# Kernel optimization log

Hardware: AMD Instinct MI355X
Metric: run time of the kernel (lower is better)

The kernel has to match this reference:

```python
import jax, jax.numpy as jnp
import numpy as np

N, C, H, W = 8, 256, 100, 252
TOPK_RATIO = 0.1
CLUSTER_RATIO = 0.125
KNN_K = 10


def setup_inputs() -> dict:
    key = jax.random.key(0)
    ks = jax.random.split(key, 4)
    x = jax.random.normal(ks[0], (N, C, H, W), jnp.float32)
    w1 = jax.random.normal(ks[1], (C, C), jnp.float32) * (1.0 / np.sqrt(C))
    b1 = jnp.zeros((C,), jnp.float32)
    w2 = jax.random.normal(ks[2], (C,), jnp.float32) * (1.0 / np.sqrt(C))
    b2 = jnp.zeros((1,), jnp.float32)
    dis_priority = jnp.ones((N, H, W), jnp.float32)
    record_len = jnp.array([4, 4], dtype=jnp.int32)
    return {"x": x, "w1": w1, "b1": b1, "w2": w2, "b2": b2,
            "dis_priority": dis_priority, "record_len": record_len}


def _layernorm(t, eps=1e-5):
    mu = jnp.mean(t, -1, keepdims=True)
    var = jnp.var(t, -1, keepdims=True)
    return (t - mu) / jnp.sqrt(var + eps)


def reference(x, w1, b1, w2, b2, dis_priority, record_len):
    HW = H * W
    S = int(HW * TOPK_RATIO)                       # sampled tokens per CAV
    K = max(int(np.ceil(S * CLUSTER_RATIO)), 1)    # DPC-KNN cluster count

    xf = x.reshape(N, C, HW)
    # SortSampler: 2layer-fc-256 score net (1x1 convs == per-pixel MLP)
    h1 = jax.nn.relu(jnp.einsum('nch,dc->ndh', xf, w1) + b1[None, :, None])
    score = jax.nn.sigmoid(jnp.einsum('nch,c->nh', h1, w2) + b2)   # [N,HW]
    score = score * dis_priority.reshape(N, HW)

    conf_topk, topk_idx = jax.lax.top_k(score, S)  # descending-sort top-k
    tokens = jnp.take_along_axis(xf, topk_idx[:, None, :], axis=2)  # [N,C,S]
    tokens = _layernorm(tokens.transpose(0, 2, 1))                  # [N,S,C]
    tokens = tokens * conf_topk[..., None]

    # --- cluster_dpc_knn (TCFormer-style DPC-KNN) ---
    sq = jnp.sum(tokens * tokens, -1)
    d2 = sq[:, :, None] + sq[:, None, :] - 2.0 * jnp.einsum('bsc,btc->bst', tokens, tokens)
    dist = jnp.sqrt(jnp.maximum(d2, 1e-12)) / np.sqrt(C)            # [N,S,S]
    neg_near, _ = jax.lax.top_k(-dist, KNN_K)                       # k nearest
    density = jnp.exp(-jnp.mean(neg_near * neg_near, -1))
    density = density + jax.random.uniform(jax.random.key(1), density.shape) * 1e-6
    mask = density[:, None, :] > density[:, :, None]
    dist_max = dist.max(axis=(1, 2), keepdims=True)
    parent_dist = jnp.where(mask, dist, dist_max).min(-1)           # [N,S]
    cscore = parent_dist * density
    _, index_down = jax.lax.top_k(cscore, K)                        # [N,K]
    dist_c = jnp.take_along_axis(dist, index_down[:, :, None], axis=1)  # [N,K,S]
    idx_cluster = jnp.argmin(dist_c, axis=1)                        # [N,S]
    bidx = jnp.arange(N)[:, None]
    idx_cluster = idx_cluster.at[bidx, index_down].set(jnp.arange(K)[None, :])

    # --- merge_tokens: confidence-weighted average per cluster ---
    flat_idx = (idx_cluster + jnp.arange(N)[:, None] * K).reshape(-1)
    wgt = conf_topk.reshape(-1)
    all_w = jax.ops.segment_sum(wgt, flat_idx, num_segments=N * K) + 1e-6
    norm_w = (wgt / all_w[flat_idx])[:, None]
    merged = jax.ops.segment_sum(tokens.reshape(-1, C) * norm_w, flat_idx,
                                 num_segments=N * K).reshape(N, K, C)

    # index_points: broadcast cluster token back to its members
    src = jnp.take_along_axis(merged, idx_cluster[..., None], axis=1)  # [N,S,C]

    # scatter sampled tokens into dense spatial grid
    out = jnp.zeros((N, C, HW), x.dtype)
    out = out.at[bidx, :, topk_idx].set(src)       # [N,S] adv idx -> [N,S,C]

    # ego CAV (first in each record group) keeps full-resolution features
    starts = jnp.concatenate([jnp.zeros((1,), jnp.int32),
                              jnp.cumsum(record_len)[:-1].astype(jnp.int32)])
    is_ego = jnp.zeros((N,), bool).at[starts].set(True)
    out = jnp.where(is_ego[:, None, None], xf, out)
    return out.reshape(N, C, H, W)
```

## Files before the change

### kernel.cpp

```cpp
#include <hip/hip_runtime.h>
#include <cstdio>
#include <cstdint>

#define NN  8
#define CCH 256
#define HWP 25200
#define SS  2520
#define KCL 315
#define KNN 10

__device__ __forceinline__ unsigned fmap(float f) {
  unsigned u = __float_as_uint(f);
  return (u & 0x80000000u) ? ~u : (u | 0x80000000u);
}
__device__ __forceinline__ float funmap(unsigned u) {
  unsigned b = (u & 0x80000000u) ? (u & 0x7fffffffu) : ~u;
  return __uint_as_float(b);
}

__global__ __launch_bounds__(256) void k_w1t(const float* __restrict__ w1, float* __restrict__ w1T) {
  __shared__ float tile[32][33];
  const int bx = blockIdx.x * 32, by = blockIdx.y * 32;
  const int tx = threadIdx.x, ty = threadIdx.y;
  for (int r = 0; r < 32; r += 8)
    tile[ty + r][tx] = w1[(by + ty + r) * CCH + bx + tx];
  __syncthreads();
  for (int r = 0; r < 32; r += 8)
    w1T[(bx + ty + r) * CCH + by + tx] = tile[tx][ty + r];
}

__global__ __launch_bounds__(256) void k_score(
    const float* __restrict__ x, const float* __restrict__ w1T,
    const float* __restrict__ b1, const float* __restrict__ w2,
    const float* __restrict__ b2, const float* __restrict__ pri,
    float* __restrict__ scores)
{
  __shared__ float Wl[16 * 256];
  __shared__ float Xl[16 * 64];
  __shared__ float red[64 * 33];
  const int n = blockIdx.y, p0 = blockIdx.x * 64, tid = threadIdx.x;
  const int dt = tid & 31, pt = tid >> 5;
  float acc[8][8];
#pragma unroll
  for (int i = 0; i < 8; ++i)
#pragma unroll
    for (int j = 0; j < 8; ++j) acc[i][j] = 0.f;

  for (int c0 = 0; c0 < CCH; c0 += 16) {
    {
      const float4* src = (const float4*)(w1T + (size_t)c0 * CCH);
      float4* dst = (float4*)Wl;
#pragma unroll
      for (int i = 0; i < 4; ++i) dst[tid + 256 * i] = src[tid + 256 * i];
    }
    {
      int kk = tid >> 4, q = tid & 15;
      int gp = p0 + 4 * q; if (gp > HWP - 4) gp = HWP - 4;
      *(float4*)&Xl[kk * 64 + 4 * q] = *(const float4*)&x[(size_t)(n * CCH + c0 + kk) * HWP + gp];
    }
    __syncthreads();
#pragma unroll
    for (int kk = 0; kk < 16; ++kk) {
      const float4 w0 = *(const float4*)&Wl[kk * 256 + 4 * dt];
      const float4 w1v = *(const float4*)&Wl[kk * 256 + 128 + 4 * dt];
      const float4 x0 = *(const float4*)&Xl[kk * 64 + 4 * pt];
      const float4 x1 = *(const float4*)&Xl[kk * 64 + 32 + 4 * pt];
      const float a[8] = {w0.x, w0.y, w0.z, w0.w, w1v.x, w1v.y, w1v.z, w1v.w};
      const float b[8] = {x0.x, x0.y, x0.z, x0.w, x1.x, x1.y, x1.z, x1.w};
#pragma unroll
      for (int di = 0; di < 8; ++di)
#pragma unroll
        for (int pj = 0; pj < 8; ++pj) acc[di][pj] += a[di] * b[pj];
    }
    __syncthreads();
  }
  float part[8];
#pragma unroll
  for (int pj = 0; pj < 8; ++pj) part[pj] = 0.f;
#pragma unroll
  for (int di = 0; di < 8; ++di) {
    int d = (di < 4) ? (4 * dt + di) : (128 + 4 * dt + di - 4);
    float bb = b1[d], wv = w2[d];
#pragma unroll
    for (int pj = 0; pj < 8; ++pj) {
      float h = acc[di][pj] + bb; h = h > 0.f ? h : 0.f;
      part[pj] += h * wv;
    }
  }
#pragma unroll
  for (int pj = 0; pj < 8; ++pj) {
    int px = (pj < 4) ? (4 * pt + pj) : (32 + 4 * pt + pj - 4);
    red[px * 33 + dt] = part[pj];
  }
  __syncthreads();
  if (tid < 64) {
    float s = b2[0];
#pragma unroll
    for (int g = 0; g < 32; ++g) s += red[tid * 33 + g];
    float sc = 1.f / (1.f + expf(-s));
    int p = p0 + tid;
    if (p < HWP) scores[n * HWP + p] = sc * pri[n * HWP + p];
  }
}

__device__ __forceinline__ void bitonic4096_desc(unsigned long long* keys, int tid) {
  for (int k = 2; k <= 4096; k <<= 1) {
    for (int j = k >> 1; j > 0; j >>= 1) {
      for (int i = tid; i < 4096; i += 1024) {
        int ixj = i ^ j;
        if (ixj > i) {
          unsigned long long a = keys[i], b = keys[ixj];
          bool up = ((i & k) == 0);
          if ((a < b) == up) { keys[i] = b; keys[ixj] = a; }
        }
      }
      __syncthreads();
    }
  }
}

__global__ __launch_bounds__(1024) void k_topk_sample(
    const float* __restrict__ scores, int* __restrict__ topk_idx, float* __restrict__ conf)
{
  __shared__ unsigned hist[256];
  __shared__ unsigned long long keys[4096];
  __shared__ unsigned sh_rank, sh_chosen;
  __shared__ int sh_cnt;
  const int n = blockIdx.x;
  const int tid = threadIdx.x;
  if (tid == 0) sh_rank = SS;
  __syncthreads();
  unsigned prefix = 0, pmask = 0;
  for (int shift = 24; shift >= 0; shift -= 8) {
    for (int b = tid; b < 256; b += 1024) hist[b] = 0;
    __syncthreads();
    for (int e = tid; e < HWP; e += 1024) {
      unsigned u = fmap(scores[n * HWP + e]);
      if ((u & pmask) == prefix) atomicAdd(&hist[(u >> shift) & 255u], 1u);
    }
    __syncthreads();
    if (tid == 0) {
      unsigned r = sh_rank, chosen = 0;
      for (int b = 255; b >= 0; --b) {
        unsigned cb = hist[b];
        if (cb < r) r -= cb; else { chosen = (unsigned)b; break; }
      }
      sh_rank = r; sh_chosen = chosen;
    }
    __syncthreads();
    prefix |= sh_chosen << shift;
    pmask  |= 0xFFu << shift;
    __syncthreads();
  }
  const unsigned uT = prefix;
  if (tid == 0) sh_cnt = 0;
  for (int i = tid; i < 4096; i += 1024) keys[i] = 0ULL;
  __syncthreads();
  for (int e = tid; e < HWP; e += 1024) {
    unsigned u = fmap(scores[n * HWP + e]);
    if (u >= uT) {
      int s = atomicAdd(&sh_cnt, 1);
      if (s < 4096) keys[s] = ((unsigned long long)u << 32) | (unsigned)(~(unsigned)e);
    }
  }
  __syncthreads();
  bitonic4096_desc(keys, tid);
  for (int t = tid; t < SS; t += 1024) {
    unsigned long long kv = keys[t];
    topk_idx[n * SS + t] = (int)(~(unsigned)kv);
    conf[n * SS + t] = funmap((unsigned)(kv >> 32));
  }
}

__device__ __forceinline__ float block_sum256(float v, float* scratch) {
#pragma unroll
  for (int o = 32; o > 0; o >>= 1) v += __shfl_down(v, o);
  int wid = threadIdx.x >> 6, lane = threadIdx.x & 63;
  if (lane == 0) scratch[wid] = v;
  __syncthreads();
  float r = scratch[0] + scratch[1] + scratch[2] + scratch[3];
  __syncthreads();
  return r;
}

__global__ __launch_bounds__(256) void k_gather_ln(
    const float* __restrict__ x, const int* __restrict__ topk_idx,
    const float* __restrict__ conf, float* __restrict__ tokens, float* __restrict__ sq)
{
  __shared__ float scratch[4];
  const int t = blockIdx.x, n = blockIdx.y, c = threadIdx.x;
  const int p = topk_idx[n * SS + t];
  float v = x[(size_t)(n * CCH + c) * HWP + p];
  float mu = block_sum256(v, scratch) * (1.f / CCH);
  float d = v - mu;
  float var = block_sum256(d * d, scratch) * (1.f / CCH);
  float inv = 1.f / sqrtf(var + 1e-5f);
  float tok = d * inv * conf[n * SS + t];
  tokens[(size_t)(n * SS + t) * CCH + c] = tok;
  float s2 = block_sum256(tok * tok, scratch);
  if (c == 0) sq[n * SS + t] = s2;
}

__global__ __launch_bounds__(256) void k_ttrans(
    const float* __restrict__ tokens, float* __restrict__ tokensT)
{
  __shared__ float tile[64][68];
  const int n = blockIdx.z, t0 = blockIdx.x * 64, cc0 = blockIdx.y * 64;
  const int tid = threadIdx.x;
  for (int l = tid; l < 1024; l += 256) {
    int tr = l >> 4, q = l & 15;
    int gt = t0 + tr;
    float4 v = {0.f, 0.f, 0.f, 0.f};
    if (gt < SS) v = *(const float4*)&tokens[(size_t)(n * SS + gt) * CCH + cc0 + 4 * q];
    *(float4*)&tile[tr][4 * q] = v;
  }
  __syncthreads();
  for (int l = tid; l < 1024; l += 256) {
    int cr = l >> 4, q = l & 15;
    int gt = t0 + 4 * q;
    if (gt <= SS - 4) {
      float4 v;
      v.x = tile[4 * q + 0][cr]; v.y = tile[4 * q + 1][cr];
      v.z = tile[4 * q + 2][cr]; v.w = tile[4 * q + 3][cr];
      *(float4*)&tokensT[(size_t)(n * CCH + cc0 + cr) * SS + gt] = v;
    }
  }
}

__global__ __launch_bounds__(256) void k_gram(
    const float* __restrict__ tokensT, const float* __restrict__ sq,
    float* __restrict__ d2, int* __restrict__ d2max)
{
  const int bi = blockIdx.y, bj = blockIdx.x, n = blockIdx.z;
  if (bj < bi) return;
  __shared__ float Al[16 * 128], Bl[16 * 128];
  __shared__ float redm[256];
  const int i0 = bi * 128, j0 = bj * 128, tid = threadIdx.x;
  const int ti = tid & 15, tj = tid >> 4;
  float acc[8][8];
#pragma unroll
  for (int i = 0; i < 8; ++i)
#pragma unroll
    for (int j = 0; j < 8; ++j) acc[i][j] = 0.f;

  for (int c0 = 0; c0 < CCH; c0 += 16) {
#pragma unroll
    for (int l0 = 0; l0 < 2; ++l0) {
      int l = threadIdx.x + 256 * l0;
      int kk = l >> 5, q = l & 31;
      size_t srow = (size_t)(n * CCH + c0 + kk) * SS;
      float4 z = {0.f, 0.f, 0.f, 0.f};
      int gi = i0 + 4 * q;
      *(float4*)&Al[kk * 128 + 4 * q] = (gi <= SS - 4) ? *(const float4*)&tokensT[srow + gi] : z;
      int gj = j0 + 4 * q;
      *(float4*)&Bl[kk * 128 + 4 * q] = (gj <= SS - 4) ? *(const float4*)&tokensT[srow + gj] : z;
    }
    __syncthreads();
#pragma unroll
    for (int kk = 0; kk < 16; ++kk) {
      const float4 a0 = *(const float4*)&Al[kk * 128 + 4 * ti];
      const float4 a1 = *(const float4*)&Al[kk * 128 + 64 + 4 * ti];
      const float4 b0 = *(const float4*)&Bl[kk * 128 + 4 * tj];
      const float4 b1 = *(const float4*)&Bl[kk * 128 + 64 + 4 * tj];
      const float a[8] = {a0.x, a0.y, a0.z, a0.w, a1.x, a1.y, a1.z, a1.w};
      const float b[8] = {b0.x, b0.y, b0.z, b0.w, b1.x, b1.y, b1.z, b1.w};
#pragma unroll
      for (int ii = 0; ii < 8; ++ii)
#pragma unroll
        for (int jj = 0; jj < 8; ++jj) acc[ii][jj] += a[ii] * b[jj];
    }
    __syncthreads();
  }
  int gi[8], gj[8];
  float sqi[8], sqj[8];
#pragma unroll
  for (int ii = 0; ii < 8; ++ii) {
    gi[ii] = i0 + ((ii < 4) ? (4 * ti + ii) : (64 + 4 * ti + ii - 4));
    sqi[ii] = (gi[ii] < SS) ? sq[n * SS + gi[ii]] : 0.f;
    gj[ii] = j0 + ((ii < 4) ? (4 * tj + ii) : (64 + 4 * tj + ii - 4));
    sqj[ii] = (gj[ii] < SS) ? sq[n * SS + gj[ii]] : 0.f;
  }
  float outv[8][8];
  float mx = -3e38f;
#pragma unroll
  for (int ii = 0; ii < 8; ++ii)
#pragma unroll
    for (int jj = 0; jj < 8; ++jj) {
      float o = sqi[ii] + sqj[jj] - 2.f * acc[ii][jj];
      outv[ii][jj] = o;
      if (gi[ii] < SS && gj[jj] < SS) mx = fmaxf(mx, o);
    }
#pragma unroll
  for (int ii = 0; ii < 8; ++ii) {
    if (gi[ii] < SS) {
      size_t row = (size_t)(n * SS + gi[ii]) * SS;
      int jb0 = j0 + 4 * tj;
      float4 o0 = {outv[ii][0], outv[ii][1], outv[ii][2], outv[ii][3]};
      *(float4*)&d2[row + jb0] = o0;
      int jb1 = j0 + 64 + 4 * tj;
      if (jb1 < SS) {
        float4 o1 = {outv[ii][4], outv[ii][5], outv[ii][6], outv[ii][7]};
        *(float4*)&d2[row + jb1] = o1;
      }
    }
  }
  if (bi != bj) {
#pragma unroll
    for (int jj = 0; jj < 8; ++jj) {
      if (gj[jj] < SS) {
        size_t row = (size_t)(n * SS + gj[jj]) * SS;
        int ib0 = i0 + 4 * ti;
        float4 m0 = {outv[0][jj], outv[1][jj], outv[2][jj], outv[3][jj]};
        *(float4*)&d2[row + ib0] = m0;
        int ib1 = i0 + 64 + 4 * ti;
        if (ib1 < SS) {
          float4 m1 = {outv[4][jj], outv[5][jj], outv[6][jj], outv[7][jj]};
          *(float4*)&d2[row + ib1] = m1;
        }
      }
    }
  }
  redm[tid] = mx; __syncthreads();
  for (int s = 128; s > 0; s >>= 1) {
    if (tid < s) redm[tid] = fmaxf(redm[tid], redm[tid + s]);
    __syncthreads();
  }
  if (tid == 0) atomicMax(&d2max[n], __float_as_int(redm[0]));
}

__global__ __launch_bounds__(256) void k_knn(
    const float* __restrict__ d2, float* __restrict__ density)
{
  const int n = blockIdx.y;
  const int w = threadIdx.x >> 6, lane = threadIdx.x & 63;
  const int i = blockIdx.x * 4 + w;
  const float* dr = &d2[(size_t)(n * SS + i) * SS];
  float s[KNN];
#pragma unroll
  for (int k = 0; k < KNN; ++k) s[k] = 3e38f;
  for (int e = lane; e < SS; e += 64) {
    float t = dr[e];
#pragma unroll
    for (int k = 0; k < KNN; ++k) {
      float lo = fminf(s[k], t);
      t = fmaxf(s[k], t);
      s[k] = lo;
    }
  }
  float sum = 0.f;
  for (int r = 0; r < KNN; ++r) {
    float m = s[0];
#pragma unroll
    for (int o = 32; o > 0; o >>= 1) m = fminf(m, __shfl_xor(m, o));
    unsigned long long msk = __ballot(s[0] == m);
    int first = __ffsll(msk) - 1;
    if (lane == first) {
#pragma unroll
      for (int k = 0; k < KNN - 1; ++k) s[k] = s[k + 1];
      s[KNN - 1] = 3e38f;
    }
    sum += fmaxf(m, 1e-12f);
  }
  if (lane == 0) density[n * SS + i] = expf(-sum * (1.f / (KNN * CCH)));
}

__global__ __launch_bounds__(256) void k_parent(
    const float* __restrict__ d2, const float* __restrict__ density,
    const int* __restrict__ d2max, float* __restrict__ cscore)
{
  __shared__ float swv[4];
  const int i = blockIdx.x, n = blockIdx.y, tid = threadIdx.x;
  const float di = density[n * SS + i];
  const float* dr = &d2[(size_t)(n * SS + i) * SS];
  float m = 3e38f;
  for (int e = tid; e < SS; e += 256) {
    float dj = density[n * SS + e];
    float v = dr[e];
    if (dj > di && v < m) m = v;
  }
#pragma unroll
  for (int o = 32; o > 0; o >>= 1) m = fminf(m, __shfl_down(m, o));
  int wid = tid >> 6, lane = tid & 63;
  if (lane == 0) swv[wid] = m;
  __syncthreads();
  if (tid == 0) {
    float mm = fminf(fminf(swv[0], swv[1]), fminf(swv[2], swv[3]));
    mm = fminf(mm, __int_as_float(d2max[n]));
    float pd = sqrtf(fmaxf(mm, 1e-12f)) * 0.0625f;
    cscore[n * SS + i] = pd * di;
  }
}

__global__ __launch_bounds__(1024) void k_topk_centers(
    const float* __restrict__ cscore, int* __restrict__ index_down)
{
  __shared__ unsigned long long keys[4096];
  const int n = blockIdx.x, tid = threadIdx.x;
  for (int i = tid; i < 4096; i += 1024) {
    unsigned long long kv = 0ULL;
    if (i < SS) kv = ((unsigned long long)fmap(cscore[n * SS + i]) << 32) | (unsigned)(~(unsigned)i);
    keys[i] = kv;
  }
  __syncthreads();
  bitonic4096_desc(keys, tid);
  for (int t = tid; t < KCL; t += 1024)
    index_down[n * KCL + t] = (int)(~(unsigned)keys[t]);
}

__global__ __launch_bounds__(256) void k_assign(
    const float* __restrict__ d2, const int* __restrict__ index_down,
    int* __restrict__ idx_cluster)
{
  const int n = blockIdx.y;
  const int i = blockIdx.x * 256 + threadIdx.x;
  if (i >= SS) return;
  float best = 3e38f; int bk = 0;
  for (int k = 0; k < KCL; ++k) {
    int r = index_down[n * KCL + k];
    float v = d2[(size_t)(n * SS + r) * SS + i];
    if (v < best) { best = v; bk = k; }
  }
  idx_cluster[n * SS + i] = bk;
}

__global__ void k_center_overwrite(const int* __restrict__ index_down, int* __restrict__ idx_cluster) {
  const int n = blockIdx.x; const int k = threadIdx.x;
  if (k < KCL) idx_cluster[n * SS + index_down[n * KCL + k]] = k;
}

__global__ __launch_bounds__(256) void k_weights(
    const int* __restrict__ idx_cluster, const float* __restrict__ conf, float* __restrict__ all_w)
{
  const int n = blockIdx.y; const int i = blockIdx.x * 256 + threadIdx.x;
  if (i >= SS) return;
  atomicAdd(&all_w[n * KCL + idx_cluster[n * SS + i]], conf[n * SS + i]);
}

__global__ __launch_bounds__(256) void k_merge(
    const int* __restrict__ idx_cluster, const float* __restrict__ conf,
    const float* __restrict__ all_w, const float* __restrict__ tokens, float* __restrict__ merged)
{
  const int t = blockIdx.x, n = blockIdx.y, c = threadIdx.x;
  const int k = idx_cluster[n * SS + t];
  const float w = conf[n * SS + t] / (all_w[n * KCL + k] + 1e-6f);
  atomicAdd(&merged[(size_t)(n * KCL + k) * CCH + c],
            tokens[(size_t)(n * SS + t) * CCH + c] * w);
}

__global__ __launch_bounds__(256) void k_kmap(
    const int* __restrict__ topk_idx, const int* __restrict__ idx_cluster, int* __restrict__ kmap)
{
  const int n = blockIdx.y; const int i = blockIdx.x * 256 + threadIdx.x;
  if (i >= SS) return;
  kmap[n * HWP + topk_idx[n * SS + i]] = idx_cluster[n * SS + i];
}

__global__ void k_ego(const int* __restrict__ record_len, int R, int* __restrict__ ego) {
  if (threadIdx.x == 0 && blockIdx.x == 0) {
    int acc = 0;
    for (int r = 0; r < R; ++r) {
      if (acc >= 0 && acc < NN) ego[acc] = 1;
      acc += record_len[r];
    }
  }
}

__global__ __launch_bounds__(256) void k_output(
    const float* __restrict__ x, const float* __restrict__ merged,
    const int* __restrict__ kmap, const int* __restrict__ ego, float* __restrict__ out)
{
  const int n = blockIdx.z, c = blockIdx.y;
  const int p4 = blockIdx.x * 256 + threadIdx.x;
  if (p4 >= HWP / 4) return;
  const size_t base = (size_t)(n * CCH + c) * HWP + 4 * p4;
  float4 v;
  if (ego[n]) {
    v = *(const float4*)&x[base];
  } else {
    int4 k4 = *(const int4*)&kmap[n * HWP + 4 * p4];
    const float* mb = &merged[(size_t)n * KCL * CCH + c];
    v.x = (k4.x >= 0) ? mb[(size_t)k4.x * CCH] : 0.f;
    v.y = (k4.y >= 0) ? mb[(size_t)k4.y * CCH] : 0.f;
    v.z = (k4.z >= 0) ? mb[(size_t)k4.z * CCH] : 0.f;
    v.w = (k4.w >= 0) ? mb[(size_t)k4.w * CCH] : 0.f;
  }
  *(float4*)&out[base] = v;
}

extern "C" void kernel_launch(void* const* d_in, const int* in_sizes, int n_in,
                              void* d_out, int out_size, void* d_ws, size_t ws_size,
                              hipStream_t stream)
{
  const float* x   = (const float*)d_in[0];
  const float* w1  = (const float*)d_in[1];
  const float* b1  = (const float*)d_in[2];
  const float* w2  = (const float*)d_in[3];
  const float* b2  = (const float*)d_in[4];
  const float* pri = (const float*)d_in[5];
  const int*   rec = (const int*)d_in[6];
  const int R = in_sizes[6];
  float* out = (float*)d_out;

  char* ws = (char*)d_ws;
  size_t off = 0;
  auto alloc = [&](size_t bytes) -> char* {
    char* p = ws + off;
    off = (off + bytes + 255) & ~(size_t)255;
    return p;
  };
  float* scores      = (float*)alloc(sizeof(float) * NN * HWP);
  int*   topk_idx    = (int*)  alloc(sizeof(int)   * NN * SS);
  float* conf        = (float*)alloc(sizeof(float) * NN * SS);
  float* tokens      = (float*)alloc(sizeof(float) * (size_t)NN * SS * CCH);
  float* tokensT     = (float*)alloc(sizeof(float) * (size_t)NN * CCH * SS);
  float* w1T         = (float*)alloc(sizeof(float) * CCH * CCH);
  float* sq          = (float*)alloc(sizeof(float) * NN * SS);
  float* density     = (float*)alloc(sizeof(float) * NN * SS);
  float* cscore      = (float*)alloc(sizeof(float) * NN * SS);
  int*   d2max       = (int*)  alloc(sizeof(int)   * NN);
  int*   index_down  = (int*)  alloc(sizeof(int)   * NN * KCL);
  int*   idx_cluster = (int*)  alloc(sizeof(int)   * NN * SS);
  float* all_w       = (float*)alloc(sizeof(float) * NN * KCL);
  float* merged      = (float*)alloc(sizeof(float) * (size_t)NN * KCL * CCH);
  int*   kmap        = (int*)  alloc(sizeof(int)   * NN * HWP);
  int*   ego         = (int*)  alloc(sizeof(int)   * NN);
  float* d2          = (float*)alloc(sizeof(float) * (size_t)NN * SS * SS);
  if (off > ws_size)
    fprintf(stderr, "ERMVP kernel: workspace too small: need %zu, have %zu\n", off, ws_size);

  hipMemsetAsync(d2max, 0, sizeof(int) * NN, stream);
  hipMemsetAsync(all_w, 0, sizeof(float) * NN * KCL, stream);
  hipMemsetAsync(merged, 0, sizeof(float) * (size_t)NN * KCL * CCH, stream);
  hipMemsetAsync(kmap, 0xFF, sizeof(int) * NN * HWP, stream);
  hipMemsetAsync(ego, 0, sizeof(int) * NN, stream);

  k_w1t<<<dim3(8, 8), dim3(32, 8), 0, stream>>>(w1, w1T);
  k_score<<<dim3((HWP + 63) / 64, NN), 256, 0, stream>>>(x, w1T, b1, w2, b2, pri, scores);
  k_topk_sample<<<NN, 1024, 0, stream>>>(scores, topk_idx, conf);
  k_gather_ln<<<dim3(SS, NN), 256, 0, stream>>>(x, topk_idx, conf, tokens, sq);
  k_ttrans<<<dim3((SS + 63) / 64, CCH / 64, NN), 256, 0, stream>>>(tokens, tokensT);
  k_gram<<<dim3(20, 20, NN), 256, 0, stream>>>(tokensT, sq, d2, d2max);
  k_knn<<<dim3(SS / 4, NN), 256, 0, stream>>>(d2, density);
  k_parent<<<dim3(SS, NN), 256, 0, stream>>>(d2, density, d2max, cscore);
  k_topk_centers<<<NN, 1024, 0, stream>>>(cscore, index_down);
  k_assign<<<dim3((SS + 255) / 256, NN), 256, 0, stream>>>(d2, index_down, idx_cluster);
  k_center_overwrite<<<NN, 320, 0, stream>>>(index_down, idx_cluster);
  k_weights<<<dim3((SS + 255) / 256, NN), 256, 0, stream>>>(idx_cluster, conf, all_w);
  k_merge<<<dim3(SS, NN), 256, 0, stream>>>(idx_cluster, conf, all_w, tokens, merged);
  k_kmap<<<dim3((SS + 255) / 256, NN), 256, 0, stream>>>(topk_idx, idx_cluster, kmap);
  k_ego<<<1, 64, 0, stream>>>(rec, R, ego);
  k_output<<<dim3((HWP / 4 + 255) / 256, CCH, NN), 256, 0, stream>>>(x, merged, kmap, ego, out);
}
```

Baseline: 1.267 ms.

## Replace bitonic sorts with radix-select compaction and fuse small clustering kernels

Both top-k kernels now skip the full 4096-element bitonic sort. They find the k-th threshold with the existing radix histogram passes, then compact the selected elements in index order using ballot/popcount prefix sums, with tie-breaking handled explicitly. The sampler also stages the score row in dynamic LDS so the histogram passes do not reread global memory. The center overwrite, weight accumulation and kmap scatter are folded into k_assign, and the ego flag is computed inline in k_output, which removes four small launches and a memset. Selected tokens and centers now come out in index order rather than score order; this relies on later stages being invariant to that permutation, apart from possible argmin tie-breaking differences.

```diff
diff --git a/kernel.cpp b/kernel.cpp
--- a/kernel.cpp
+++ b/kernel.cpp
@@ -12,10 +12,6 @@
 __device__ __forceinline__ unsigned fmap(float f) {
   unsigned u = __float_as_uint(f);
   return (u & 0x80000000u) ? ~u : (u | 0x80000000u);
-}
-__device__ __forceinline__ float funmap(unsigned u) {
-  unsigned b = (u & 0x80000000u) ? (u & 0x7fffffffu) : ~u;
-  return __uint_as_float(b);
 }
 
 __global__ __launch_bounds__(256) void k_w1t(const float* __restrict__ w1, float* __restrict__ w1T) {
@@ -103,39 +99,31 @@
   }
 }
 
-__device__ __forceinline__ void bitonic4096_desc(unsigned long long* keys, int tid) {
-  for (int k = 2; k <= 4096; k <<= 1) {
-    for (int j = k >> 1; j > 0; j >>= 1) {
-      for (int i = tid; i < 4096; i += 1024) {
-        int ixj = i ^ j;
-        if (ixj > i) {
-          unsigned long long a = keys[i], b = keys[ixj];
-          bool up = ((i & k) == 0);
-          if ((a < b) == up) { keys[i] = b; keys[ixj] = a; }
-        }
-      }
-      __syncthreads();
-    }
-  }
-}
-
 __global__ __launch_bounds__(1024) void k_topk_sample(
     const float* __restrict__ scores, int* __restrict__ topk_idx, float* __restrict__ conf)
 {
+  extern __shared__ float sc_lds[];
   __shared__ unsigned hist[256];
-  __shared__ unsigned long long keys[4096];
+  __shared__ int wcnt[16], woff[16];
+  __shared__ int sh_base, sh_tbase, sh_ngt;
   __shared__ unsigned sh_rank, sh_chosen;
-  __shared__ int sh_cnt;
-  const int n = blockIdx.x;
-  const int tid = threadIdx.x;
-  if (tid == 0) sh_rank = SS;
-  __syncthreads();
+  const int n = blockIdx.x, tid = threadIdx.x;
+  const int lane = tid & 63, w = tid >> 6;
+
+  {
+    const float4* src = (const float4*)(scores + (size_t)n * HWP);
+    float4* dst = (float4*)sc_lds;
+    for (int i = tid; i < HWP / 4; i += 1024) dst[i] = src[i];
+  }
+  if (tid == 0) { sh_rank = SS; sh_ngt = 0; sh_base = 0; sh_tbase = 0; }
+  __syncthreads();
+
   unsigned prefix = 0, pmask = 0;
   for (int shift = 24; shift >= 0; shift -= 8) {
-    for (int b = tid; b < 256; b += 1024) hist[b] = 0;
+    if (tid < 256) hist[tid] = 0;
     __syncthreads();
     for (int e = tid; e < HWP; e += 1024) {
-      unsigned u = fmap(scores[n * HWP + e]);
+      unsigned u = fmap(sc_lds[e]);
       if ((u & pmask) == prefix) atomicAdd(&hist[(u >> shift) & 255u], 1u);
     }
     __syncthreads();
@@ -153,22 +141,50 @@
     __syncthreads();
   }
   const unsigned uT = prefix;
-  if (tid == 0) sh_cnt = 0;
-  for (int i = tid; i < 4096; i += 1024) keys[i] = 0ULL;
-  __syncthreads();
-  for (int e = tid; e < HWP; e += 1024) {
-    unsigned u = fmap(scores[n * HWP + e]);
-    if (u >= uT) {
-      int s = atomicAdd(&sh_cnt, 1);
-      if (s < 4096) keys[s] = ((unsigned long long)u << 32) | (unsigned)(~(unsigned)e);
-    }
-  }
-  __syncthreads();
-  bitonic4096_desc(keys, tid);
-  for (int t = tid; t < SS; t += 1024) {
-    unsigned long long kv = keys[t];
-    topk_idx[n * SS + t] = (int)(~(unsigned)kv);
-    conf[n * SS + t] = funmap((unsigned)(kv >> 32));
+
+  {
+    int myg = 0;
+    for (int e = tid; e < HWP; e += 1024) myg += (fmap(sc_lds[e]) > uT);
+#pragma unroll
+    for (int o = 32; o > 0; o >>= 1) myg += __shfl_down(myg, o);
+    if (lane == 0) atomicAdd(&sh_ngt, myg);
+  }
+  __syncthreads();
+  const int T = SS - sh_ngt;
+
+  for (int c0 = 0; c0 < HWP; c0 += 1024) {
+    const int e = c0 + tid;
+    const bool valid = e < HWP;
+    const float s = valid ? sc_lds[e] : 0.f;
+    const unsigned u = valid ? fmap(s) : 0u;
+    const bool tie = valid && (u == uT);
+    const bool gt  = valid && (u > uT);
+    unsigned long long mt = __ballot(tie);
+    if (lane == 0) wcnt[w] = __popcll(mt);
+    __syncthreads();
+    if (tid == 0) {
+      int run = sh_tbase;
+      for (int q = 0; q < 16; ++q) { woff[q] = run; run += wcnt[q]; }
+      sh_tbase = run;
+    }
+    __syncthreads();
+    const int trank = woff[w] + __popcll(mt & ((1ULL << lane) - 1ULL));
+    const bool sel = gt || (tie && trank < T);
+    unsigned long long ms = __ballot(sel);
+    if (lane == 0) wcnt[w] = __popcll(ms);
+    __syncthreads();
+    if (tid == 0) {
+      int run = sh_base;
+      for (int q = 0; q < 16; ++q) { woff[q] = run; run += wcnt[q]; }
+      sh_base = run;
+    }
+    __syncthreads();
+    if (sel) {
+      int pos = woff[w] + __popcll(ms & ((1ULL << lane) - 1ULL));
+      topk_idx[n * SS + pos] = e;
+      conf[n * SS + pos] = s;
+    }
+    __syncthreads();
   }
 }
 
@@ -394,46 +410,105 @@
 __global__ __launch_bounds__(1024) void k_topk_centers(
     const float* __restrict__ cscore, int* __restrict__ index_down)
 {
-  __shared__ unsigned long long keys[4096];
+  __shared__ float cs_lds[SS];
+  __shared__ unsigned hist[256];
+  __shared__ int wcnt[16], woff[16];
+  __shared__ int sh_base, sh_tbase, sh_ngt;
+  __shared__ unsigned sh_rank, sh_chosen;
   const int n = blockIdx.x, tid = threadIdx.x;
-  for (int i = tid; i < 4096; i += 1024) {
-    unsigned long long kv = 0ULL;
-    if (i < SS) kv = ((unsigned long long)fmap(cscore[n * SS + i]) << 32) | (unsigned)(~(unsigned)i);
-    keys[i] = kv;
-  }
-  __syncthreads();
-  bitonic4096_desc(keys, tid);
-  for (int t = tid; t < KCL; t += 1024)
-    index_down[n * KCL + t] = (int)(~(unsigned)keys[t]);
+  const int lane = tid & 63, w = tid >> 6;
+
+  for (int e = tid; e < SS; e += 1024) cs_lds[e] = cscore[n * SS + e];
+  if (tid == 0) { sh_rank = KCL; sh_ngt = 0; sh_base = 0; sh_tbase = 0; }
+  __syncthreads();
+
+  unsigned prefix = 0, pmask = 0;
+  for (int shift = 24; shift >= 0; shift -= 8) {
+    if (tid < 256) hist[tid] = 0;
+    __syncthreads();
+    for (int e = tid; e < SS; e += 1024) {
+      unsigned u = fmap(cs_lds[e]);
+      if ((u & pmask) == prefix) atomicAdd(&hist[(u >> shift) & 255u], 1u);
+    }
+    __syncthreads();
+    if (tid == 0) {
+      unsigned r = sh_rank, chosen = 0;
+      for (int b = 255; b >= 0; --b) {
+        unsigned cb = hist[b];
+        if (cb < r) r -= cb; else { chosen = (unsigned)b; break; }
+      }
+      sh_rank = r; sh_chosen = chosen;
+    }
+    __syncthreads();
+    prefix |= sh_chosen << shift;
+    pmask  |= 0xFFu << shift;
+    __syncthreads();
+  }
+  const unsigned uT = prefix;
+
+  {
+    int myg = 0;
+    for (int e = tid; e < SS; e += 1024) myg += (fmap(cs_lds[e]) > uT);
+#pragma unroll
+    for (int o = 32; o > 0; o >>= 1) myg += __shfl_down(myg, o);
+    if (lane == 0) atomicAdd(&sh_ngt, myg);
+  }
+  __syncthreads();
+  const int T = KCL - sh_ngt;
+
+  for (int c0 = 0; c0 < SS; c0 += 1024) {
+    const int e = c0 + tid;
+    const bool valid = e < SS;
+    const unsigned u = valid ? fmap(cs_lds[e]) : 0u;
+    const bool tie = valid && (u == uT);
+    const bool gt  = valid && (u > uT);
+    unsigned long long mt = __ballot(tie);
+    if (lane == 0) wcnt[w] = __popcll(mt);
+    __syncthreads();
+    if (tid == 0) {
+      int run = sh_tbase;
+      for (int q = 0; q < 16; ++q) { woff[q] = run; run += wcnt[q]; }
+      sh_tbase = run;
+    }
+    __syncthreads();
+    const int trank = woff[w] + __popcll(mt & ((1ULL << lane) - 1ULL));
+    const bool sel = gt || (tie && trank < T);
+    unsigned long long ms = __ballot(sel);
+    if (lane == 0) wcnt[w] = __popcll(ms);
+    __syncthreads();
+    if (tid == 0) {
+      int run = sh_base;
+      for (int q = 0; q < 16; ++q) { woff[q] = run; run += wcnt[q]; }
+      sh_base = run;
+    }
+    __syncthreads();
+    if (sel) {
+      int pos = woff[w] + __popcll(ms & ((1ULL << lane) - 1ULL));
+      index_down[n * KCL + pos] = e;
+    }
+    __syncthreads();
+  }
 }
 
 __global__ __launch_bounds__(256) void k_assign(
     const float* __restrict__ d2, const int* __restrict__ index_down,
-    int* __restrict__ idx_cluster)
+    const float* __restrict__ conf, const int* __restrict__ topk_idx,
+    int* __restrict__ idx_cluster, float* __restrict__ all_w, int* __restrict__ kmap)
 {
   const int n = blockIdx.y;
   const int i = blockIdx.x * 256 + threadIdx.x;
   if (i >= SS) return;
-  float best = 3e38f; int bk = 0;
+  float best = 3e38f; int bk = 0, forced = -1;
   for (int k = 0; k < KCL; ++k) {
     int r = index_down[n * KCL + k];
+    if (r == i) forced = k;
     float v = d2[(size_t)(n * SS + r) * SS + i];
     if (v < best) { best = v; bk = k; }
   }
+  if (forced >= 0) bk = forced;
   idx_cluster[n * SS + i] = bk;
-}
-
-__global__ void k_center_overwrite(const int* __restrict__ index_down, int* __restrict__ idx_cluster) {
-  const int n = blockIdx.x; const int k = threadIdx.x;
-  if (k < KCL) idx_cluster[n * SS + index_down[n * KCL + k]] = k;
-}
-
-__global__ __launch_bounds__(256) void k_weights(
-    const int* __restrict__ idx_cluster, const float* __restrict__ conf, float* __restrict__ all_w)
-{
-  const int n = blockIdx.y; const int i = blockIdx.x * 256 + threadIdx.x;
-  if (i >= SS) return;
-  atomicAdd(&all_w[n * KCL + idx_cluster[n * SS + i]], conf[n * SS + i]);
+  atomicAdd(&all_w[n * KCL + bk], conf[n * SS + i]);
+  kmap[n * HWP + topk_idx[n * SS + i]] = bk;
 }
 
 __global__ __launch_bounds__(256) void k_merge(
@@ -447,34 +522,22 @@
             tokens[(size_t)(n * SS + t) * CCH + c] * w);
 }
 
-__global__ __launch_bounds__(256) void k_kmap(
-    const int* __restrict__ topk_idx, const int* __restrict__ idx_cluster, int* __restrict__ kmap)
-{
-  const int n = blockIdx.y; const int i = blockIdx.x * 256 + threadIdx.x;
-  if (i >= SS) return;
-  kmap[n * HWP + topk_idx[n * SS + i]] = idx_cluster[n * SS + i];
-}
-
-__global__ void k_ego(const int* __restrict__ record_len, int R, int* __restrict__ ego) {
-  if (threadIdx.x == 0 && blockIdx.x == 0) {
-    int acc = 0;
-    for (int r = 0; r < R; ++r) {
-      if (acc >= 0 && acc < NN) ego[acc] = 1;
-      acc += record_len[r];
-    }
-  }
-}
-
 __global__ __launch_bounds__(256) void k_output(
     const float* __restrict__ x, const float* __restrict__ merged,
-    const int* __restrict__ kmap, const int* __restrict__ ego, float* __restrict__ out)
+    const int* __restrict__ kmap, const int* __restrict__ rec, int R,
+    float* __restrict__ out)
 {
   const int n = blockIdx.z, c = blockIdx.y;
   const int p4 = blockIdx.x * 256 + threadIdx.x;
   if (p4 >= HWP / 4) return;
+  bool ego = false;
+  {
+    int acc = 0;
+    for (int r = 0; r < R; ++r) { if (acc == n) ego = true; acc += rec[r]; }
+  }
   const size_t base = (size_t)(n * CCH + c) * HWP + 4 * p4;
   float4 v;
-  if (ego[n]) {
+  if (ego) {
     v = *(const float4*)&x[base];
   } else {
     int4 k4 = *(const int4*)&kmap[n * HWP + 4 * p4];
@@ -523,7 +586,6 @@
   float* all_w       = (float*)alloc(sizeof(float) * NN * KCL);
   float* merged      = (float*)alloc(sizeof(float) * (size_t)NN * KCL * CCH);
   int*   kmap        = (int*)  alloc(sizeof(int)   * NN * HWP);
-  int*   ego         = (int*)  alloc(sizeof(int)   * NN);
   float* d2          = (float*)alloc(sizeof(float) * (size_t)NN * SS * SS);
   if (off > ws_size)
     fprintf(stderr, "ERMVP kernel: workspace too small: need %zu, have %zu\n", off, ws_size);
@@ -532,22 +594,18 @@
   hipMemsetAsync(all_w, 0, sizeof(float) * NN * KCL, stream);
   hipMemsetAsync(merged, 0, sizeof(float) * (size_t)NN * KCL * CCH, stream);
   hipMemsetAsync(kmap, 0xFF, sizeof(int) * NN * HWP, stream);
-  hipMemsetAsync(ego, 0, sizeof(int) * NN, stream);
 
   k_w1t<<<dim3(8, 8), dim3(32, 8), 0, stream>>>(w1, w1T);
   k_score<<<dim3((HWP + 63) / 64, NN), 256, 0, stream>>>(x, w1T, b1, w2, b2, pri, scores);
-  k_topk_sample<<<NN, 1024, 0, stream>>>(scores, topk_idx, conf);
+  k_topk_sample<<<NN, 1024, sizeof(float) * HWP, stream>>>(scores, topk_idx, conf);
   k_gather_ln<<<dim3(SS, NN), 256, 0, stream>>>(x, topk_idx, conf, tokens, sq);
   k_ttrans<<<dim3((SS + 63) / 64, CCH / 64, NN), 256, 0, stream>>>(tokens, tokensT);
   k_gram<<<dim3(20, 20, NN), 256, 0, stream>>>(tokensT, sq, d2, d2max);
   k_knn<<<dim3(SS / 4, NN), 256, 0, stream>>>(d2, density);
   k_parent<<<dim3(SS, NN), 256, 0, stream>>>(d2, density, d2max, cscore);
   k_topk_centers<<<NN, 1024, 0, stream>>>(cscore, index_down);
-  k_assign<<<dim3((SS + 255) / 256, NN), 256, 0, stream>>>(d2, index_down, idx_cluster);
-  k_center_overwrite<<<NN, 320, 0, stream>>>(index_down, idx_cluster);
-  k_weights<<<dim3((SS + 255) / 256, NN), 256, 0, stream>>>(idx_cluster, conf, all_w);
+  k_assign<<<dim3((SS + 255) / 256, NN), 256, 0, stream>>>(d2, index_down, conf, topk_idx,
+                                                           idx_cluster, all_w, kmap);
   k_merge<<<dim3(SS, NN), 256, 0, stream>>>(idx_cluster, conf, all_w, tokens, merged);
-  k_kmap<<<dim3((SS + 255) / 256, NN), 256, 0, stream>>>(topk_idx, idx_cluster, kmap);
-  k_ego<<<1, 64, 0, stream>>>(rec, R, ego);
-  k_output<<<dim3((HWP / 4 + 255) / 256, CCH, NN), 256, 0, stream>>>(x, merged, kmap, ego, out);
-}
+  k_output<<<dim3((HWP / 4 + 255) / 256, CCH, NN), 256, 0, stream>>>(x, merged, kmap, rec, R, out);
+}
```

Result: faster. 1.211 ms (-4.4%).
